# Performance work log

Measured on AMD Instinct MI355X. Metric: run time of the kernel, lower is better.

Reference implementation:

```python
import jax, jax.numpy as jnp
import numpy as np

B, D, L, N = 16, 256, 4096, 4096
MAX_SPAN = 64


def setup_inputs() -> dict:
    key = jax.random.key(0)
    k1, k2, k3 = jax.random.split(key, 3)
    features = jax.random.normal(k1, (B, D, L), dtype=jnp.float32)
    # TOI spans: start in [0, L - MAX_SPAN), length in [1, MAX_SPAN]
    start = jax.random.randint(k2, (B, N), 0, L - MAX_SPAN, dtype=jnp.int32)
    length = jax.random.randint(k3, (B, N), 1, MAX_SPAN + 1, dtype=jnp.int32)
    tois = jnp.stack([start, start + length], axis=-1)  # [B, N, 2]
    return {"features": features, "tois": tois}


def _pool_one(feat, toi):
    # feat: [D, L], toi: [N, 2] -> [N, 3*D]
    start = toi[:, 0]
    end = toi[:, 1]
    # cumsum with zero-padding column: [D, L+1]
    cs = jnp.concatenate(
        [jnp.zeros((feat.shape[0], 1), dtype=feat.dtype), jnp.cumsum(feat, axis=1)],
        axis=1,
    )
    span_len = (end - start).astype(feat.dtype)
    avg = (cs[:, end] - cs[:, start]) / span_len          # [D, N]
    head = feat[:, start]                                  # [D, N]
    tail = feat[:, end - 1]                                # [D, N]
    return jnp.concatenate([head, avg, tail], axis=0).T    # [N, 3*D]


def reference(features, tois):
    # features: [B, D, L] float32, tois: [B, N, 2] int32
    pooled = jax.vmap(_pool_one)(features, tois)           # [B, N, 3*D]
    out = pooled.reshape(-1, pooled.shape[-1])             # [B*N, 3*D]
    n = tois.shape[1]
    counts = jnp.cumsum(jnp.full((tois.shape[0],), n, dtype=jnp.int32))
    return out, counts
```

## Files before the change

### kernel.cpp

```cpp
#include <hip/hip_runtime.h>

constexpr int B = 16;
constexpr int D = 256;
constexpr int L = 4096;
constexpr int N = 4096;
constexpr int TS = 64;
constexpr int NTL = L / TS;
constexpr int NBIN = B * NTL;
constexpr int WIN = 128;
constexpr int SD = 65;

typedef float v4f __attribute__((ext_vector_type(4)));


__global__ __launch_bounds__(256) void q_hist(const int* __restrict__ tois,
                                              int* __restrict__ cnt) {
    __shared__ int h[NTL];
    int tid = threadIdx.x;
    if (tid < NTL) h[tid] = 0;
    __syncthreads();
    int q = blockIdx.x * 256 + tid;
    int s = tois[q * 2];
    atomicAdd(&h[s >> 6], 1);
    __syncthreads();
    int b = blockIdx.x >> 4;
    if (tid < NTL) { int v = h[tid]; if (v) atomicAdd(&cnt[b * NTL + tid], v); }
}

__global__ __launch_bounds__(1024) void q_offsets(const int* __restrict__ cnt,
                                                  int* __restrict__ off) {
    __shared__ int wt[16];
    int tid = threadIdx.x;
    int v = cnt[tid];
    int incl = v;
    #pragma unroll
    for (int o = 1; o < 64; o <<= 1) {
        int u = __shfl_up(incl, o, 64);
        if ((tid & 63) >= o) incl += u;
    }
    if ((tid & 63) == 63) wt[tid >> 6] = incl;
    __syncthreads();
    if (tid == 0) {
        int a = 0;
        #pragma unroll
        for (int i = 0; i < 16; ++i) { int t2 = wt[i]; wt[i] = a; a += t2; }
        off[NBIN] = a;
    }
    __syncthreads();
    off[tid] = wt[tid >> 6] + incl - v;
}

__global__ __launch_bounds__(256) void q_scatter(const int* __restrict__ tois,
                                                 const int* __restrict__ off,
                                                 int* __restrict__ cur,
                                                 int* __restrict__ qlist,
                                                 float* __restrict__ out) {
    int tid = threadIdx.x;
    int q = blockIdx.x * 256 + tid;
    int s = tois[q * 2];
    int b = q >> 12;
    int bin = b * NTL + (s >> 6);
    int pos = atomicAdd(&cur[bin], 1);
    qlist[off[bin] + pos] = q;
    if (q < B) out[(size_t)B * N * (3 * D) + q] = (float)((q + 1) * N);
}

__global__ __launch_bounds__(256, 4) void pool(const float* __restrict__ feat,
                                               const int* __restrict__ tois,
                                               const int* __restrict__ off,
                                               const int* __restrict__ qlist,
                                               float* __restrict__ out) {
    __shared__ float cs[WIN][SD];
    __shared__ float qtot[4][64];
    __shared__ float qoff[4][64];

    int bid  = blockIdx.x;
    int nbid = (bid & 7) * ((int)gridDim.x >> 3) + (bid >> 3);
    int dq = nbid & 3;
    int t  = (nbid >> 2) & 63;
    int b  = nbid >> 8;
    int bin = b * NTL + t;
    int qs0 = off[bin];
    int nq  = off[bin + 1] - qs0;
    if (nq == 0) return;

    int tid = threadIdx.x, lane = tid & 63, wv = tid >> 6;
    int d0 = dq * 64, l0 = t * TS;

    const float* fb = feat + ((size_t)(b * D + d0)) * L + l0;
    #pragma unroll
    for (int k = 0; k < 8; ++k) {
        int g = k * 256 + tid;
        int r = g >> 5, cc = g & 31;
        v4f v = *(const v4f*)(fb + (size_t)r * L + cc * 4);
        cs[cc * 4 + 0][r] = v.x;
        cs[cc * 4 + 1][r] = v.y;
        cs[cc * 4 + 2][r] = v.z;
        cs[cc * 4 + 3][r] = v.w;
    }
    __syncthreads();

    {
        float c = 0.f;
        #pragma unroll
        for (int i = 0; i < 32; ++i) {
            int l = wv * 32 + i;
            float v = cs[l][lane];
            cs[l][lane] = c;
            c += v;
        }
        qtot[wv][lane] = c;
    }
    __syncthreads();
    if (tid < 64) {
        float o = 0.f;
        #pragma unroll
        for (int qr = 0; qr < 4; ++qr) { float v = qtot[qr][tid]; qoff[qr][tid] = o; o += v; }
    }
    __syncthreads();
    if (wv) {
        float o = qoff[wv][lane];
        #pragma unroll
        for (int i = 0; i < 32; ++i) cs[wv * 32 + i][lane] += o;
    }
    __syncthreads();

    const int2* tp = (const int2*)tois;
    for (int it = wv; it < nq; it += 4) {
        int q = qlist[qs0 + it];
        int2 se = tp[q];
        int si = se.x - l0;
        int ei = se.y - l0;
        float a0 = cs[si][lane];
        float a1 = cs[si + 1][lane];
        float e0 = cs[ei][lane];
        float e1 = cs[ei - 1][lane];
        float inv = 1.0f / (float)(se.y - se.x);
        float head = a1 - a0;
        float avg  = (e0 - a0) * inv;
        float tail = e0 - e1;
        float* orow = out + (size_t)q * (3 * D) + d0 + lane;
        __builtin_nontemporal_store(head, orow);
        __builtin_nontemporal_store(avg,  orow + D);
        __builtin_nontemporal_store(tail, orow + 2 * D);
    }
}

__global__ __launch_bounds__(256) void pool_direct(const float* __restrict__ feat,
                                                   const int* __restrict__ tois,
                                                   float* __restrict__ out) {
    int gw   = (blockIdx.x * blockDim.x + threadIdx.x) >> 6;
    int lane = threadIdx.x & 63;
    if (gw >= B * N) return;
    int b = gw >> 12;
    int s = tois[gw * 2 + 0];
    int e = tois[gw * 2 + 1];
    float inv = 1.0f / (float)(e - s);
    float* orow = out + (size_t)gw * (3 * D);
    #pragma unroll
    for (int c = 0; c < 4; ++c) {
        int d = c * 64 + lane;
        const float* f = feat + ((size_t)(b * D + d)) * L;
        float sum = 0.f;
        for (int j = s; j < e; ++j) sum += f[j];
        orow[d]         = f[s];
        orow[D + d]     = sum * inv;
        orow[2 * D + d] = f[e - 1];
    }
    if (gw == 0 && lane < B)
        out[(size_t)B * N * (3 * D) + lane] = (float)((lane + 1) * N);
}

extern "C" void kernel_launch(void* const* d_in, const int* in_sizes, int n_in,
                              void* d_out, int out_size, void* d_ws, size_t ws_size,
                              hipStream_t stream) {
    const float* feat = (const float*)d_in[0];
    const int*   tois = (const int*)d_in[1];
    float*       out  = (float*)d_out;

    int* cnt   = (int*)d_ws;
    int* cur   = cnt + NBIN;
    int* off   = cur + NBIN;
    int* qlist = off + NBIN + 1;
    const size_t need = (size_t)(NBIN * 2 + NBIN + 1 + B * N) * sizeof(int);

    if (ws_size >= need) {
        hipMemsetAsync(cnt, 0, (size_t)NBIN * 2 * sizeof(int), stream);
        q_hist   <<<B * N / 256, 256, 0, stream>>>(tois, cnt);
        q_offsets<<<1, 1024, 0, stream>>>(cnt, off);
        q_scatter<<<B * N / 256, 256, 0, stream>>>(tois, off, cur, qlist, out);
        pool     <<<B * (D / 64) * NTL, 256, 0, stream>>>(feat, tois, off, qlist, out);
    } else {
        pool_direct<<<B * N / 4, 256, 0, stream>>>(feat, tois, out);
    }
}
```

Measured before the change: 270.0 us.

## Fuse query binning into pool kernel with per-block scan of span list

Drops the separate histogram, offset-scan and scatter kernels and the workspace memset. Instead, each pool block scans its batch's spans in chunks of 1024 and builds a local list of those whose start falls in its tile, using a shared-memory atomic counter and packed query/offset/length words. The tile loop covers only 63 tiles, relying on the generator's bound that start < L - 64. The shared buffer is now laid out [d][l] with an odd stride and loaded with scalar reads, where it was [l][d] with vector loads. The aim is to remove launch overhead and global atomics, at the cost of every block rereading all 32KB of spans for its batch.

```diff
diff --git a/kernel.cpp b/kernel.cpp
--- a/kernel.cpp
+++ b/kernel.cpp
@@ -1,102 +1,42 @@
 #include <hip/hip_runtime.h>
 
-constexpr int B = 16;
-constexpr int D = 256;
-constexpr int L = 4096;
-constexpr int N = 4096;
-constexpr int TS = 64;
-constexpr int NTL = L / TS;
-constexpr int NBIN = B * NTL;
+constexpr int B   = 16;
+constexpr int D   = 256;
+constexpr int L   = 4096;
+constexpr int N   = 4096;
+constexpr int TS  = 64;
+constexpr int NTU = 63;
 constexpr int WIN = 128;
-constexpr int SD = 65;
-
-typedef float v4f __attribute__((ext_vector_type(4)));
-
-
-__global__ __launch_bounds__(256) void q_hist(const int* __restrict__ tois,
-                                              int* __restrict__ cnt) {
-    __shared__ int h[NTL];
-    int tid = threadIdx.x;
-    if (tid < NTL) h[tid] = 0;
-    __syncthreads();
-    int q = blockIdx.x * 256 + tid;
-    int s = tois[q * 2];
-    atomicAdd(&h[s >> 6], 1);
-    __syncthreads();
-    int b = blockIdx.x >> 4;
-    if (tid < NTL) { int v = h[tid]; if (v) atomicAdd(&cnt[b * NTL + tid], v); }
-}
-
-__global__ __launch_bounds__(1024) void q_offsets(const int* __restrict__ cnt,
-                                                  int* __restrict__ off) {
-    __shared__ int wt[16];
-    int tid = threadIdx.x;
-    int v = cnt[tid];
-    int incl = v;
-    #pragma unroll
-    for (int o = 1; o < 64; o <<= 1) {
-        int u = __shfl_up(incl, o, 64);
-        if ((tid & 63) >= o) incl += u;
-    }
-    if ((tid & 63) == 63) wt[tid >> 6] = incl;
-    __syncthreads();
-    if (tid == 0) {
-        int a = 0;
-        #pragma unroll
-        for (int i = 0; i < 16; ++i) { int t2 = wt[i]; wt[i] = a; a += t2; }
-        off[NBIN] = a;
-    }
-    __syncthreads();
-    off[tid] = wt[tid >> 6] + incl - v;
-}
-
-__global__ __launch_bounds__(256) void q_scatter(const int* __restrict__ tois,
-                                                 const int* __restrict__ off,
-                                                 int* __restrict__ cur,
-                                                 int* __restrict__ qlist,
-                                                 float* __restrict__ out) {
-    int tid = threadIdx.x;
-    int q = blockIdx.x * 256 + tid;
-    int s = tois[q * 2];
-    int b = q >> 12;
-    int bin = b * NTL + (s >> 6);
-    int pos = atomicAdd(&cur[bin], 1);
-    qlist[off[bin] + pos] = q;
-    if (q < B) out[(size_t)B * N * (3 * D) + q] = (float)((q + 1) * N);
-}
+constexpr int SDL = 129;
+constexpr int QCH = 1024;
 
 __global__ __launch_bounds__(256, 4) void pool(const float* __restrict__ feat,
                                                const int* __restrict__ tois,
-                                               const int* __restrict__ off,
-                                               const int* __restrict__ qlist,
                                                float* __restrict__ out) {
-    __shared__ float cs[WIN][SD];
+    __shared__ float cs[64][SDL];
     __shared__ float qtot[4][64];
     __shared__ float qoff[4][64];
+    __shared__ int   lq[QCH];
+    __shared__ int   lcnt;
 
     int bid  = blockIdx.x;
     int nbid = (bid & 7) * ((int)gridDim.x >> 3) + (bid >> 3);
     int dq = nbid & 3;
-    int t  = (nbid >> 2) & 63;
-    int b  = nbid >> 8;
-    int bin = b * NTL + t;
-    int qs0 = off[bin];
-    int nq  = off[bin + 1] - qs0;
-    if (nq == 0) return;
-
+    int tb = nbid >> 2;
+    int t  = tb % NTU;
+    int b  = tb / NTU;
     int tid = threadIdx.x, lane = tid & 63, wv = tid >> 6;
     int d0 = dq * 64, l0 = t * TS;
 
+    if (bid == 0 && tid < B)
+        out[(size_t)B * N * (3 * D) + tid] = (float)((tid + 1) * N);
+
     const float* fb = feat + ((size_t)(b * D + d0)) * L + l0;
     #pragma unroll
-    for (int k = 0; k < 8; ++k) {
+    for (int k = 0; k < 32; ++k) {
         int g = k * 256 + tid;
-        int r = g >> 5, cc = g & 31;
-        v4f v = *(const v4f*)(fb + (size_t)r * L + cc * 4);
-        cs[cc * 4 + 0][r] = v.x;
-        cs[cc * 4 + 1][r] = v.y;
-        cs[cc * 4 + 2][r] = v.z;
-        cs[cc * 4 + 3][r] = v.w;
+        int d = g >> 7, l = g & 127;
+        cs[d][l] = fb[(size_t)d * L + l];
     }
     __syncthreads();
 
@@ -105,8 +45,8 @@
         #pragma unroll
         for (int i = 0; i < 32; ++i) {
             int l = wv * 32 + i;
-            float v = cs[l][lane];
-            cs[l][lane] = c;
+            float v = cs[lane][l];
+            cs[lane][l] = c;
             c += v;
         }
         qtot[wv][lane] = c;
@@ -115,60 +55,56 @@
     if (tid < 64) {
         float o = 0.f;
         #pragma unroll
-        for (int qr = 0; qr < 4; ++qr) { float v = qtot[qr][tid]; qoff[qr][tid] = o; o += v; }
+        for (int q4 = 0; q4 < 4; ++q4) { float v = qtot[q4][tid]; qoff[q4][tid] = o; o += v; }
     }
     __syncthreads();
     if (wv) {
         float o = qoff[wv][lane];
         #pragma unroll
-        for (int i = 0; i < 32; ++i) cs[wv * 32 + i][lane] += o;
+        for (int i = 0; i < 32; ++i) cs[lane][wv * 32 + i] += o;
     }
-    __syncthreads();
 
-    const int2* tp = (const int2*)tois;
-    for (int it = wv; it < nq; it += 4) {
-        int q = qlist[qs0 + it];
-        int2 se = tp[q];
-        int si = se.x - l0;
-        int ei = se.y - l0;
-        float a0 = cs[si][lane];
-        float a1 = cs[si + 1][lane];
-        float e0 = cs[ei][lane];
-        float e1 = cs[ei - 1][lane];
-        float inv = 1.0f / (float)(se.y - se.x);
-        float head = a1 - a0;
-        float avg  = (e0 - a0) * inv;
-        float tail = e0 - e1;
-        float* orow = out + (size_t)q * (3 * D) + d0 + lane;
-        __builtin_nontemporal_store(head, orow);
-        __builtin_nontemporal_store(avg,  orow + D);
-        __builtin_nontemporal_store(tail, orow + 2 * D);
+    const int4* tp4 = (const int4*)tois + ((size_t)b * N >> 1);
+    for (int ch = 0; ch < N / QCH; ++ch) {
+        __syncthreads();
+        if (tid == 0) lcnt = 0;
+        __syncthreads();
+        #pragma unroll
+        for (int j = 0; j < 2; ++j) {
+            int idx2 = ch * (QCH / 2) + j * 256 + tid;
+            int4 v = tp4[idx2];
+            int ql0 = idx2 * 2;
+            if ((v.x >> 6) == t) {
+                int pos = atomicAdd(&lcnt, 1);
+                lq[pos] = (b * N + ql0) | ((v.x - l0) << 16) | ((v.y - v.x) << 22);
+            }
+            if ((v.z >> 6) == t) {
+                int pos = atomicAdd(&lcnt, 1);
+                lq[pos] = (b * N + ql0 + 1) | ((v.z - l0) << 16) | ((v.w - v.z) << 22);
+            }
+        }
+        __syncthreads();
+        int n = lcnt;
+        for (int it = wv; it < n; it += 4) {
+            int p   = lq[it];
+            int q   = p & 0xFFFF;
+            int si  = (p >> 16) & 63;
+            int len = (unsigned)p >> 22;
+            int ei  = si + len;
+            float a0 = cs[lane][si];
+            float a1 = cs[lane][si + 1];
+            float e0 = cs[lane][ei];
+            float e1 = cs[lane][ei - 1];
+            float inv  = 1.0f / (float)len;
+            float head = a1 - a0;
+            float avg  = (e0 - a0) * inv;
+            float tail = e0 - e1;
+            float* orow = out + (size_t)q * (3 * D) + d0 + lane;
+            __builtin_nontemporal_store(head, orow);
+            __builtin_nontemporal_store(avg,  orow + D);
+            __builtin_nontemporal_store(tail, orow + 2 * D);
+        }
     }
-}
-
-__global__ __launch_bounds__(256) void pool_direct(const float* __restrict__ feat,
-                                                   const int* __restrict__ tois,
-                                                   float* __restrict__ out) {
-    int gw   = (blockIdx.x * blockDim.x + threadIdx.x) >> 6;
-    int lane = threadIdx.x & 63;
-    if (gw >= B * N) return;
-    int b = gw >> 12;
-    int s = tois[gw * 2 + 0];
-    int e = tois[gw * 2 + 1];
-    float inv = 1.0f / (float)(e - s);
-    float* orow = out + (size_t)gw * (3 * D);
-    #pragma unroll
-    for (int c = 0; c < 4; ++c) {
-        int d = c * 64 + lane;
-        const float* f = feat + ((size_t)(b * D + d)) * L;
-        float sum = 0.f;
-        for (int j = s; j < e; ++j) sum += f[j];
-        orow[d]         = f[s];
-        orow[D + d]     = sum * inv;
-        orow[2 * D + d] = f[e - 1];
-    }
-    if (gw == 0 && lane < B)
-        out[(size_t)B * N * (3 * D) + lane] = (float)((lane + 1) * N);
 }
 
 extern "C" void kernel_launch(void* const* d_in, const int* in_sizes, int n_in,
@@ -177,20 +113,7 @@
     const float* feat = (const float*)d_in[0];
     const int*   tois = (const int*)d_in[1];
     float*       out  = (float*)d_out;
+    (void)d_ws; (void)ws_size;
 
-    int* cnt   = (int*)d_ws;
-    int* cur   = cnt + NBIN;
-    int* off   = cur + NBIN;
-    int* qlist = off + NBIN + 1;
-    const size_t need = (size_t)(NBIN * 2 + NBIN + 1 + B * N) * sizeof(int);
-
-    if (ws_size >= need) {
-        hipMemsetAsync(cnt, 0, (size_t)NBIN * 2 * sizeof(int), stream);
-        q_hist   <<<B * N / 256, 256, 0, stream>>>(tois, cnt);
-        q_offsets<<<1, 1024, 0, stream>>>(cnt, off);
-        q_scatter<<<B * N / 256, 256, 0, stream>>>(tois, off, cur, qlist, out);
-        pool     <<<B * (D / 64) * NTL, 256, 0, stream>>>(feat, tois, off, qlist, out);
-    } else {
-        pool_direct<<<B * N / 4, 256, 0, stream>>>(feat, tois, out);
-    }
+    pool<<<B * NTU * 4, 256, 0, stream>>>(feat, tois, out);
 }
```

After: 263.1 us. 2.6% less time.
